# Kernel tuning notes

Hardware: AMD Instinct MI355X
Metric: run time of the kernel (lower is better)

## Reference

```python
import jax, jax.numpy as jnp
import numpy as np

IN_SIZE = 128
OUT_SIZE = 128
N = IN_SIZE * OUT_SIZE  # num_nets = 16384
H = 5                   # subnetwork hidden width
B = 2048                # batch


def setup_inputs() -> dict:
    key = jax.random.key(0)
    k_x, k0, k1, k2 = jax.random.split(key, 4)
    x = jax.random.normal(k_x, (B, IN_SIZE), dtype=jnp.float32)
    # init scaling mirrors _init_scaled_weights: std*0.1, last layer uses in_dim*input_size
    s0 = np.float32(np.sqrt(2.0 / 1.0) * 0.1)
    s1 = np.float32(np.sqrt(2.0 / H) * 0.1)
    s2 = np.float32(np.sqrt(2.0 / (H * IN_SIZE)) * 0.1)
    W0 = jax.random.normal(k0, (N, H, 1), dtype=jnp.float32) * s0
    W1 = jax.random.normal(k1, (N, H, H), dtype=jnp.float32) * s1
    W2 = jax.random.normal(k2, (N, 1, H), dtype=jnp.float32) * s2
    b0 = jnp.zeros((N, H, 1), dtype=jnp.float32)
    b1 = jnp.zeros((N, H, 1), dtype=jnp.float32)
    b2 = jnp.zeros((N, 1, 1), dtype=jnp.float32)
    return {"x": x, "W0": W0, "b0": b0, "W1": W1, "b1": b1, "W2": W2, "b2": b2}


def reference(x, W0, b0, W1, b1, W2, b2):
    bsz = x.shape[0]
    # x.T repeat_interleave(output_size, dim=0).unsqueeze(1): (N, 1, B)
    h = jnp.repeat(x.T, OUT_SIZE, axis=0)[:, None, :]
    h = jax.nn.silu(jnp.einsum('noi,nib->nob', W0, h) + b0)  # (N, H, B)
    h = jax.nn.silu(jnp.einsum('noi,nib->nob', W1, h) + b1)  # (N, H, B)
    h = jnp.einsum('noi,nib->nob', W2, h) + b2               # (N, 1, B)
    h = h.reshape(IN_SIZE, OUT_SIZE, bsz)
    return h.sum(axis=0).T  # (B, OUT_SIZE)
```

## Files before the change

kernel.cpp:

```cpp
#include <hip/hip_runtime.h>
#include <math.h>

#define H 5
#define IN_SIZE 128
#define OUT_SIZE 128
#define BATCH 2048

#define DEG 20
#define NC (DEG + 1)
#define KNOD 32
#define ARANGE 5.5f
#define AINV (1.0f / 5.5f)

#define KTOT (IN_SIZE * NC)
#define WS_MFMA ((size_t)OUT_SIZE * KTOT * 2)

#define CPAD 2816
#define WS_F32 ((size_t)IN_SIZE * CPAD * sizeof(float))

typedef __attribute__((ext_vector_type(8))) short bf16x8;
typedef __attribute__((ext_vector_type(4))) float f32x4;

__device__ __forceinline__ unsigned short f2bf(float f) {
    unsigned int u = __float_as_uint(f);
    return (unsigned short)((u + 0x7FFF + ((u >> 16) & 1)) >> 16);
}

__global__ __launch_bounds__(256, 4) void fit_bf16_kernel(
    const float* __restrict__ W0, const float* __restrict__ b0,
    const float* __restrict__ W1, const float* __restrict__ b1,
    const float* __restrict__ W2, const float* __restrict__ b2,
    unsigned short* __restrict__ ct, float* __restrict__ out)
{
    __shared__ float sw[368];
    __shared__ float ybuf[8][KNOD];
    const int tid = threadIdx.x;
    const int n0  = blockIdx.x * 8;

    if (tid < 128)
        out[(size_t)blockIdx.x * 128 + tid] = 0.0f;

    for (int idx = tid; idx < 368; idx += 256) {
        float v;
        if      (idx <  40) v = W0[n0 * 5  + idx];
        else if (idx <  80) v = b0[n0 * 5  + (idx - 40)];
        else if (idx < 280) v = W1[n0 * 25 + (idx - 80)];
        else if (idx < 320) v = b1[n0 * 5  + (idx - 280)];
        else if (idx < 360) v = W2[n0 * 5  + (idx - 320)];
        else                v = b2[n0 + (idx - 360)];
        sw[idx] = v;
    }
    __syncthreads();

    const int net8 = tid >> 5;
    const int k    = tid & 31;
    const int n    = n0 + net8;
    const float* w0r = sw + net8 * 5;
    const float* b0r = sw + 40  + net8 * 5;
    const float* w1r = sw + 80  + net8 * 25;
    const float* b1r = sw + 280 + net8 * 5;
    const float* w2r = sw + 320 + net8 * 5;
    const float  b2s = sw[360 + net8];

    const float theta = (k + 0.5f) * (float)(M_PI / KNOD);
    const float xv = ARANGE * __cosf(theta);

    float h1[H];
    #pragma unroll
    for (int j = 0; j < H; ++j) {
        float p = fmaf(w0r[j], xv, b0r[j]);
        h1[j] = p / (1.0f + __expf(-p));
    }
    float h2[H];
    #pragma unroll
    for (int kk = 0; kk < H; ++kk) {
        float p = b1r[kk];
        #pragma unroll
        for (int j = 0; j < H; ++j)
            p = fmaf(w1r[kk * H + j], h1[j], p);
        h2[kk] = p / (1.0f + __expf(-p));
    }
    float y = b2s;
    #pragma unroll
    for (int kk = 0; kk < H; ++kk)
        y = fmaf(w2r[kk], h2[kk], y);

    ybuf[net8][k] = y;
    __syncthreads();

    if (k < NC) {
        float s = 0.0f;
        for (int kk = 0; kk < KNOD; ++kk) {
            float ang = (float)k * ((kk + 0.5f) * (float)(M_PI / KNOD));
            s += ybuf[net8][kk] * __cosf(ang);
        }
        s *= (k == 0) ? (1.0f / KNOD) : (2.0f / KNOD);
        const int i = n >> 7;
        const int o = n & 127;
        ct[(size_t)o * KTOT + i * NC + k] = f2bf(s);
    }
}

#define LDB 360

__global__ __launch_bounds__(256, 2) void gemm_fused_kernel(
    const float* __restrict__ x,
    const unsigned short* __restrict__ Ct,
    float* __restrict__ out)
{
    __shared__ __align__(16) unsigned short Bs[64 * LDB];
    __shared__ __align__(16) unsigned short As[32 * LDB];

    const int tid = threadIdx.x;
    const int mt = blockIdx.x;
    const int oh = blockIdx.y;
    const int kz = blockIdx.z;
    const int kbase = kz * 336;
    const int i0 = kz * 16;
    const int bb = mt * 32;

    {
        const int o = tid >> 2, c = tid & 3;
        const unsigned short* src = Ct + (size_t)(oh * 64 + o) * KTOT + kbase;
        unsigned short* drow = Bs + o * LDB;
        #pragma unroll
        for (int j = 0; j < 11; ++j) {
            const int kloc = c * 88 + j * 8;
            float4 v = make_float4(0.f, 0.f, 0.f, 0.f);
            if (kloc + 8 <= 336) v = *(const float4*)(src + kloc);
            *(float4*)(drow + kloc) = v;
        }
    }

    {
        const int b  = tid & 31;
        const int s0 = tid >> 5;
        #pragma unroll
        for (int q = 0; q < 2; ++q) {
            const int iloc = s0 + q * 8;
            const float t = x[(size_t)(bb + b) * IN_SIZE + i0 + iloc] * AINV;
            unsigned short* dst = As + b * LDB + iloc * NC;
            float Tm = 1.0f, Tc = t;
            const float t2 = t + t;
            dst[0] = 0x3F80;
            dst[1] = f2bf(t);
            #pragma unroll
            for (int k = 2; k < NC; ++k) {
                float Tn = fmaf(t2, Tc, -Tm);
                Tm = Tc; Tc = Tn;
                dst[k] = f2bf(Tn);
            }
            As[b * LDB + 336 + iloc] = 0;
        }
    }
    __syncthreads();

    const int lane = tid & 63, w = tid >> 6;
    const int wm = w >> 1, wn = w & 1;
    const int l16 = lane & 15, lg = lane >> 4;

    const unsigned short* aptr  = As + (wm * 16 + l16) * LDB + lg * 8;
    const unsigned short* bptr0 = Bs + (wn * 32 + l16) * LDB + lg * 8;
    const unsigned short* bptr1 = bptr0 + 16 * LDB;

    f32x4 acc0 = {0.f, 0.f, 0.f, 0.f};
    f32x4 acc1 = {0.f, 0.f, 0.f, 0.f};

    #pragma unroll
    for (int ks = 0; ks < 11; ++ks) {
        bf16x8 a   = *(const bf16x8*)(aptr  + ks * 32);
        bf16x8 b0v = *(const bf16x8*)(bptr0 + ks * 32);
        bf16x8 b1v = *(const bf16x8*)(bptr1 + ks * 32);
        acc0 = __builtin_amdgcn_mfma_f32_16x16x32_bf16(a, b0v, acc0, 0, 0, 0);
        acc1 = __builtin_amdgcn_mfma_f32_16x16x32_bf16(a, b1v, acc1, 0, 0, 0);
    }

    const int orow = bb + wm * 16 + lg * 4;
    const int ocol = oh * 64 + wn * 32 + l16;
    #pragma unroll
    for (int r = 0; r < 4; ++r) {
        atomicAdd(&out[(size_t)(orow + r) * OUT_SIZE + ocol],      acc0[r]);
        atomicAdd(&out[(size_t)(orow + r) * OUT_SIZE + ocol + 16], acc1[r]);
    }
}

__global__ __launch_bounds__(256, 4) void fit_kernel(
    const float* __restrict__ W0, const float* __restrict__ b0,
    const float* __restrict__ W1, const float* __restrict__ b1,
    const float* __restrict__ W2, const float* __restrict__ b2,
    float* __restrict__ coef)
{
    __shared__ float sw[368];
    __shared__ float ybuf[8][KNOD];
    const int tid = threadIdx.x;
    const int n0  = blockIdx.x * 8;

    for (int idx = tid; idx < 368; idx += 256) {
        float v;
        if      (idx <  40) v = W0[n0 * 5  + idx];
        else if (idx <  80) v = b0[n0 * 5  + (idx - 40)];
        else if (idx < 280) v = W1[n0 * 25 + (idx - 80)];
        else if (idx < 320) v = b1[n0 * 5  + (idx - 280)];
        else if (idx < 360) v = W2[n0 * 5  + (idx - 320)];
        else                v = b2[n0 + (idx - 360)];
        sw[idx] = v;
    }
    __syncthreads();

    const int net8 = tid >> 5;
    const int k    = tid & 31;
    const int n    = n0 + net8;
    const float* w0r = sw + net8 * 5;
    const float* b0r = sw + 40  + net8 * 5;
    const float* w1r = sw + 80  + net8 * 25;
    const float* b1r = sw + 280 + net8 * 5;
    const float* w2r = sw + 320 + net8 * 5;
    const float  b2s = sw[360 + net8];

    const float theta = (k + 0.5f) * (float)(M_PI / KNOD);
    const float xv = ARANGE * __cosf(theta);

    float h1[H];
    #pragma unroll
    for (int j = 0; j < H; ++j) {
        float p = fmaf(w0r[j], xv, b0r[j]);
        h1[j] = p / (1.0f + __expf(-p));
    }
    float h2[H];
    #pragma unroll
    for (int kk = 0; kk < H; ++kk) {
        float p = b1r[kk];
        #pragma unroll
        for (int j = 0; j < H; ++j)
            p = fmaf(w1r[kk * H + j], h1[j], p);
        h2[kk] = p / (1.0f + __expf(-p));
    }
    float y = b2s;
    #pragma unroll
    for (int kk = 0; kk < H; ++kk)
        y = fmaf(w2r[kk], h2[kk], y);

    ybuf[net8][k] = y;
    __syncthreads();

    const int i = n >> 7;
    const int o = n & 127;
    if (k < NC) {
        float s = 0.0f;
        for (int kk = 0; kk < KNOD; ++kk) {
            float ang = (float)k * ((kk + 0.5f) * (float)(M_PI / KNOD));
            s += ybuf[net8][kk] * __cosf(ang);
        }
        s *= (k == 0) ? (1.0f / KNOD) : (2.0f / KNOD);
        coef[(size_t)i * CPAD + k * OUT_SIZE + o] = s;
    } else if (k == NC) {
        coef[(size_t)i * CPAD + NC * OUT_SIZE + o] = 0.0f;
    }
}

__global__ __launch_bounds__(256, 2) void eval_kernel(
    const float* __restrict__ x, const float* __restrict__ coef,
    float* __restrict__ out)
{
    __shared__ __align__(16) float A[16 * NC * 32];
    __shared__ __align__(16) float Bb[2][CPAD];

    const int tid = threadIdx.x;
    const int bb  = blockIdx.x * 32;
    const int i0  = blockIdx.y * 16;

    {
        const int b  = tid & 31;
        const int s0 = tid >> 5;
        #pragma unroll
        for (int q = 0; q < 2; ++q) {
            const int isub = s0 + q * 8;
            float t  = x[(size_t)(bb + b) * IN_SIZE + i0 + isub] * AINV;
            float t2 = t + t;
            float* ap = A + (isub * NC) * 32 + b;
            float Tm = 1.0f, Tc = t;
            ap[0]  = 1.0f;
            ap[32] = t;
            #pragma unroll
            for (int k = 2; k < NC; ++k) {
                float Tn = fmaf(t2, Tc, -Tm);
                Tm = Tc; Tc = Tn;
                ap[k * 32] = Tn;
            }
        }
    }

    float r[11];
    {
        const float* cb = coef + (size_t)i0 * CPAD;
        #pragma unroll
        for (int j = 0; j < 11; ++j) r[j] = cb[tid + 256 * j];
        #pragma unroll
        for (int j = 0; j < 11; ++j) Bb[0][tid + 256 * j] = r[j];
    }
    __syncthreads();

    const int w  = tid >> 6;
    const int ty = (tid >> 3) & 7;
    const int tx = tid & 7;
    const int rb = ty * 4;
    const int ob = w * 32 + tx * 4;

    float acc[4][4] = {};

    #pragma unroll 1
    for (int isub = 0; isub < 16; ++isub) {
        const int cur = isub & 1;
        if (isub + 1 < 16) {
            const float* cb = coef + (size_t)(i0 + isub + 1) * CPAD;
            #pragma unroll
            for (int j = 0; j < 11; ++j) r[j] = cb[tid + 256 * j];
        }
        const float* Ab = A + (isub * NC) * 32;
        const float* Bp = Bb[cur];
        #pragma unroll
        for (int k = 0; k < NC; ++k) {
            float4 a4 = *(const float4*)(Ab + k * 32 + rb);
            float4 b4 = *(const float4*)(Bp + k * OUT_SIZE + ob);
            float av[4] = {a4.x, a4.y, a4.z, a4.w};
            float bv[4] = {b4.x, b4.y, b4.z, b4.w};
            #pragma unroll
            for (int rr = 0; rr < 4; ++rr)
                #pragma unroll
                for (int cc = 0; cc < 4; ++cc)
                    acc[rr][cc] = fmaf(av[rr], bv[cc], acc[rr][cc]);
        }
        if (isub + 1 < 16) {
            float* Bn = Bb[cur ^ 1];
            #pragma unroll
            for (int j = 0; j < 11; ++j) Bn[tid + 256 * j] = r[j];
        }
        __syncthreads();
    }

    #pragma unroll
    for (int rr = 0; rr < 4; ++rr) {
        float* orow = out + (size_t)(bb + rb + rr) * OUT_SIZE + ob;
        #pragma unroll
        for (int cc = 0; cc < 4; ++cc)
            atomicAdd(&orow[cc], acc[rr][cc]);
    }
}

#define ICHUNK 64
#define WSTRIDE 52

__device__ __forceinline__ float silu9(float p) {
    const float c3 = -0.33333333333333f;
    const float c5 =  0.13333333333333f;
    const float c7 = -0.05396825396825f;
    const float c9 =  0.02186948853616f;
    float u  = 0.5f * p;
    float uc = fminf(fmaxf(u, -1.25f), 1.25f);
    float t  = uc * uc;
    float g  = fmaf(t, c9, c7);
    g = fmaf(t, g, c5);
    g = fmaf(t, g, c3);
    g = fmaf(t, g, 1.0f);
    return fmaf(u, uc * g, u);
}
__device__ __forceinline__ float silu5(float p) {
    const float c3 = -0.33333333333333f;
    const float c5 =  0.13333333333333f;
    float u = 0.5f * p;
    float t = u * u;
    float g = fmaf(t, c5, c3);
    g = fmaf(t, g, 1.0f);
    return fmaf(u, u * g, u);
}

__global__ __launch_bounds__(256, 8) void mlpkan_fallback(
    const float* __restrict__ x,
    const float* __restrict__ W0, const float* __restrict__ b0,
    const float* __restrict__ W1, const float* __restrict__ b1,
    const float* __restrict__ W2, const float* __restrict__ b2,
    float* __restrict__ out)
{
    __shared__ float w[ICHUNK * WSTRIDE];
    const int o  = blockIdx.x;
    const int i0 = blockIdx.z * ICHUNK;

    for (int idx = threadIdx.x; idx < ICHUNK * WSTRIDE; idx += 256) {
        int il = idx / WSTRIDE;
        int f  = idx - il * WSTRIDE;
        int n  = (i0 + il) * OUT_SIZE + o;
        float v = 0.0f;
        if (f < 5)                   v = W0[n * 5 + f];
        else if (f < 10)             v = b0[n * 5 + (f - 5)];
        else if (f >= 12 && f < 37)  v = W1[n * 25 + (f - 12)];
        else if (f >= 37 && f < 42)  v = b1[n * 5 + (f - 37)];
        else if (f >= 44 && f < 49)  v = W2[n * 5 + (f - 44)];
        else if (f == 49)            v = b2[n];
        w[idx] = v;
    }
    __syncthreads();

    const int b = blockIdx.y * 256 + threadIdx.x;
    const float* xrow = x + b * IN_SIZE + i0;
    float acc = 0.0f;

    #pragma unroll 1
    for (int i = 0; i < ICHUNK; i += 4) {
        float4 xv = *(const float4*)(xrow + i);
        float xs[4] = {xv.x, xv.y, xv.z, xv.w};
        #pragma unroll
        for (int ii = 0; ii < 4; ++ii) {
            const float4* q = (const float4*)(w + (i + ii) * WSTRIDE);
            const float xi = xs[ii];
            float g0[12];
            #pragma unroll
            for (int t = 0; t < 3; ++t) *(float4*)(g0 + 4 * t) = q[t];
            float h1[H];
            #pragma unroll
            for (int j = 0; j < H; ++j)
                h1[j] = silu9(fmaf(g0[j], xi, g0[5 + j]));
            float g1[32];
            #pragma unroll
            for (int t = 0; t < 8; ++t) *(float4*)(g1 + 4 * t) = q[3 + t];
            float h2[H];
            #pragma unroll
            for (int k = 0; k < H; ++k) {
                float p = g1[25 + k];
                #pragma unroll
                for (int j = 0; j < H; ++j)
                    p = fmaf(g1[5 * k + j], h1[j], p);
                h2[k] = silu5(p);
            }
            float g2[8];
            #pragma unroll
            for (int t = 0; t < 2; ++t) *(float4*)(g2 + 4 * t) = q[11 + t];
            float y = g2[5];
            #pragma unroll
            for (int k = 0; k < H; ++k)
                y = fmaf(g2[k], h2[k], y);
            acc += y;
        }
    }
    atomicAdd(&out[b * OUT_SIZE + o], acc);
}

extern "C" void kernel_launch(void* const* d_in, const int* in_sizes, int n_in,
                              void* d_out, int out_size, void* d_ws, size_t ws_size,
                              hipStream_t stream) {
    const float* x  = (const float*)d_in[0];
    const float* W0 = (const float*)d_in[1];
    const float* b0 = (const float*)d_in[2];
    const float* W1 = (const float*)d_in[3];
    const float* b1 = (const float*)d_in[4];
    const float* W2 = (const float*)d_in[5];
    const float* b2 = (const float*)d_in[6];
    float* out = (float*)d_out;

    if (ws_size >= WS_MFMA && d_ws != nullptr) {
        unsigned short* Ct = (unsigned short*)d_ws;
        fit_bf16_kernel<<<dim3(IN_SIZE * OUT_SIZE / 8), dim3(256), 0, stream>>>(
            W0, b0, W1, b1, W2, b2, Ct, out);
        gemm_fused_kernel<<<dim3(BATCH / 32, 2, 8), dim3(256), 0, stream>>>(
            x, Ct, out);
    } else if (ws_size >= WS_F32 && d_ws != nullptr) {
        float* coef = (float*)d_ws;
        hipMemsetAsync(out, 0, (size_t)out_size * sizeof(float), stream);
        fit_kernel<<<dim3(IN_SIZE * OUT_SIZE / 8), dim3(256), 0, stream>>>(
            W0, b0, W1, b1, W2, b2, coef);
        eval_kernel<<<dim3(BATCH / 32, IN_SIZE / 16), dim3(256), 0, stream>>>(
            x, coef, out);
    } else {
        hipMemsetAsync(out, 0, (size_t)out_size * sizeof(float), stream);
        dim3 grid(OUT_SIZE, BATCH / 256, IN_SIZE / ICHUNK);
        mlpkan_fallback<<<grid, dim3(256), 0, stream>>>(x, W0, b0, W1, b1, W2, b2, out);
    }
}
```

Measured before the change: 89.05 us.

## Pad coefficient rows to 22 and loop two K-chunks per GEMM block

Coefficient storage is padded to 22 bf16 per input so each 16-input K chunk is 352 elements and 16-byte aligned, which removes the bounds check on the B-tile load. Each GEMM block now handles two K chunks in a loop, halving the z grid and the number of atomicAdd passes into the output. The Chebyshev A-tile is written as packed 32-bit bf16 pairs instead of single shorts. The cost is an extra barrier per block and less grid parallelism.

```diff
diff --git a/kernel.cpp b/kernel.cpp
--- a/kernel.cpp
+++ b/kernel.cpp
@@ -12,8 +12,8 @@
 #define ARANGE 5.5f
 #define AINV (1.0f / 5.5f)
 
-#define KTOT (IN_SIZE * NC)
-#define WS_MFMA ((size_t)OUT_SIZE * KTOT * 2)
+#define KROW 2816
+#define WS_MFMA ((size_t)OUT_SIZE * KROW * 2)
 
 #define CPAD 2816
 #define WS_F32 ((size_t)IN_SIZE * CPAD * sizeof(float))
@@ -24,6 +24,9 @@
 __device__ __forceinline__ unsigned short f2bf(float f) {
     unsigned int u = __float_as_uint(f);
     return (unsigned short)((u + 0x7FFF + ((u >> 16) & 1)) >> 16);
+}
+__device__ __forceinline__ unsigned int packbf(float lo, float hi) {
+    return (unsigned int)f2bf(lo) | ((unsigned int)f2bf(hi) << 16);
 }
 
 __global__ __launch_bounds__(256, 4) void fit_bf16_kernel(
@@ -88,6 +91,8 @@
     ybuf[net8][k] = y;
     __syncthreads();
 
+    const int i = n >> 7;
+    const int o = n & 127;
     if (k < NC) {
         float s = 0.0f;
         for (int kk = 0; kk < KNOD; ++kk) {
@@ -95,9 +100,9 @@
             s += ybuf[net8][kk] * __cosf(ang);
         }
         s *= (k == 0) ? (1.0f / KNOD) : (2.0f / KNOD);
-        const int i = n >> 7;
-        const int o = n & 127;
-        ct[(size_t)o * KTOT + i * NC + k] = f2bf(s);
+        ct[(size_t)o * KROW + i * 22 + k] = f2bf(s);
+    } else if (k == NC) {
+        ct[(size_t)o * KROW + i * 22 + NC] = 0;
     }
 }
 
@@ -114,46 +119,7 @@
     const int tid = threadIdx.x;
     const int mt = blockIdx.x;
     const int oh = blockIdx.y;
-    const int kz = blockIdx.z;
-    const int kbase = kz * 336;
-    const int i0 = kz * 16;
     const int bb = mt * 32;
-
-    {
-        const int o = tid >> 2, c = tid & 3;
-        const unsigned short* src = Ct + (size_t)(oh * 64 + o) * KTOT + kbase;
-        unsigned short* drow = Bs + o * LDB;
-        #pragma unroll
-        for (int j = 0; j < 11; ++j) {
-            const int kloc = c * 88 + j * 8;
-            float4 v = make_float4(0.f, 0.f, 0.f, 0.f);
-            if (kloc + 8 <= 336) v = *(const float4*)(src + kloc);
-            *(float4*)(drow + kloc) = v;
-        }
-    }
-
-    {
-        const int b  = tid & 31;
-        const int s0 = tid >> 5;
-        #pragma unroll
-        for (int q = 0; q < 2; ++q) {
-            const int iloc = s0 + q * 8;
-            const float t = x[(size_t)(bb + b) * IN_SIZE + i0 + iloc] * AINV;
-            unsigned short* dst = As + b * LDB + iloc * NC;
-            float Tm = 1.0f, Tc = t;
-            const float t2 = t + t;
-            dst[0] = 0x3F80;
-            dst[1] = f2bf(t);
-            #pragma unroll
-            for (int k = 2; k < NC; ++k) {
-                float Tn = fmaf(t2, Tc, -Tm);
-                Tm = Tc; Tc = Tn;
-                dst[k] = f2bf(Tn);
-            }
-            As[b * LDB + 336 + iloc] = 0;
-        }
-    }
-    __syncthreads();
 
     const int lane = tid & 63, w = tid >> 6;
     const int wm = w >> 1, wn = w & 1;
@@ -167,12 +133,56 @@
     f32x4 acc1 = {0.f, 0.f, 0.f, 0.f};
 
     #pragma unroll
-    for (int ks = 0; ks < 11; ++ks) {
-        bf16x8 a   = *(const bf16x8*)(aptr  + ks * 32);
-        bf16x8 b0v = *(const bf16x8*)(bptr0 + ks * 32);
-        bf16x8 b1v = *(const bf16x8*)(bptr1 + ks * 32);
-        acc0 = __builtin_amdgcn_mfma_f32_16x16x32_bf16(a, b0v, acc0, 0, 0, 0);
-        acc1 = __builtin_amdgcn_mfma_f32_16x16x32_bf16(a, b1v, acc1, 0, 0, 0);
+    for (int s = 0; s < 2; ++s) {
+        const int kz = blockIdx.z * 2 + s;
+        const int kbase = kz * 352;
+        const int i0 = kz * 16;
+
+        if (s) __syncthreads();
+
+        {
+            const int o = tid >> 2, c = tid & 3;
+            const unsigned short* src = Ct + (size_t)(oh * 64 + o) * KROW + kbase;
+            unsigned short* drow = Bs + o * LDB;
+            #pragma unroll
+            for (int j = 0; j < 11; ++j) {
+                const int kloc = c * 88 + j * 8;
+                *(float4*)(drow + kloc) = *(const float4*)(src + kloc);
+            }
+        }
+
+        {
+            const int b  = tid & 31;
+            const int s0 = tid >> 5;
+            unsigned int* A32 = (unsigned int*)(As + b * LDB);
+            #pragma unroll
+            for (int q = 0; q < 2; ++q) {
+                const int iloc = s0 + q * 8;
+                const float t = x[(size_t)(bb + b) * IN_SIZE + i0 + iloc] * AINV;
+                float Tv[NC];
+                Tv[0] = 1.0f;
+                Tv[1] = t;
+                const float t2 = t + t;
+                #pragma unroll
+                for (int k = 2; k < NC; ++k)
+                    Tv[k] = fmaf(t2, Tv[k - 1], -Tv[k - 2]);
+                unsigned int* dst = A32 + iloc * 11;
+                #pragma unroll
+                for (int j = 0; j < 10; ++j)
+                    dst[j] = packbf(Tv[2 * j], Tv[2 * j + 1]);
+                dst[10] = packbf(Tv[20], 0.0f);
+            }
+        }
+        __syncthreads();
+
+        #pragma unroll
+        for (int ks = 0; ks < 11; ++ks) {
+            bf16x8 a   = *(const bf16x8*)(aptr  + ks * 32);
+            bf16x8 b0v = *(const bf16x8*)(bptr0 + ks * 32);
+            bf16x8 b1v = *(const bf16x8*)(bptr1 + ks * 32);
+            acc0 = __builtin_amdgcn_mfma_f32_16x16x32_bf16(a, b0v, acc0, 0, 0, 0);
+            acc1 = __builtin_amdgcn_mfma_f32_16x16x32_bf16(a, b1v, acc1, 0, 0, 0);
+        }
     }
 
     const int orow = bb + wm * 16 + lg * 4;
@@ -460,7 +470,7 @@
         unsigned short* Ct = (unsigned short*)d_ws;
         fit_bf16_kernel<<<dim3(IN_SIZE * OUT_SIZE / 8), dim3(256), 0, stream>>>(
             W0, b0, W1, b1, W2, b2, Ct, out);
-        gemm_fused_kernel<<<dim3(BATCH / 32, 2, 8), dim3(256), 0, stream>>>(
+        gemm_fused_kernel<<<dim3(BATCH / 32, 2, 4), dim3(256), 0, stream>>>(
             x, Ct, out);
     } else if (ws_size >= WS_F32 && d_ws != nullptr) {
         float* coef = (float*)d_ws;
```

Measured after the change: 81.63 us, median of 2. 8.3% less time.
